# Kernel optimization log

Measured on AMD Instinct MI355X. Metric: run time of the kernel, lower is better.

## Reference

```python
import jax, jax.numpy as jnp
import numpy as np

N_NODES = 50000


def _sage_conv(x, src, dst, Wl, bl, Wr):
    # mean aggregation of source-node features into target nodes
    agg = jax.ops.segment_sum(x[src], dst, num_segments=N_NODES)      # [N, C]
    deg = jax.ops.segment_sum(jnp.ones_like(src, dtype=x.dtype), dst,
                              num_segments=N_NODES)                   # [N]
    mean = agg / jnp.maximum(deg, 1.0)[:, None]
    # PyG SAGEConv: lin_l(aggr) (with bias) + lin_r(x) (no bias)
    return mean @ Wl.T + bl + x @ Wr.T


def setup_inputs() -> dict:
    key = jax.random.key(0)
    ks = jax.random.split(key, 8)
    C = 128
    E = 600000
    scale = 1.0 / np.sqrt(C)
    x = jax.random.normal(ks[0], (N_NODES, C), dtype=jnp.float32)
    edge_index = jax.random.randint(ks[1], (2, E), 0, N_NODES, dtype=jnp.int64)
    Wl1 = jax.random.normal(ks[2], (C, C), dtype=jnp.float32) * scale
    bl1 = jnp.zeros((C,), dtype=jnp.float32)
    Wr1 = jax.random.normal(ks[3], (C, C), dtype=jnp.float32) * scale
    Wl2 = jax.random.normal(ks[4], (C, C), dtype=jnp.float32) * scale
    bl2 = jnp.zeros((C,), dtype=jnp.float32)
    Wr2 = jax.random.normal(ks[5], (C, C), dtype=jnp.float32) * scale
    return {"x": x, "edge_index": edge_index, "Wl1": Wl1, "bl1": bl1,
            "Wr1": Wr1, "Wl2": Wl2, "bl2": bl2, "Wr2": Wr2}


def reference(x, edge_index, Wl1, bl1, Wr1, Wl2, bl2, Wr2):
    src, dst = edge_index[0], edge_index[1]
    h = _sage_conv(x, src, dst, Wl1, bl1, Wr1)
    h = jax.nn.relu(h)
    out = _sage_conv(h, src, dst, Wl2, bl2, Wr2)
    return out
```

## Files before the change

### kernel.cpp

```cpp
#include <hip/hip_runtime.h>
#include <hip/hip_bf16.h>

#define N_NODES 50000
#define C 128
#define NPAD 50176
#define NTILES (NPAD / 16)
#define GEMM_BLOCKS (NTILES / 8)
#define XPREP_BLOCKS 3125
#define WPREP_BLOCKS 256
#define CAP 48

typedef short bf16x8 __attribute__((ext_vector_type(8)));
typedef float f32x4 __attribute__((ext_vector_type(4)));

__device__ __forceinline__ unsigned short f2bf(float f) {
    unsigned int u = __float_as_uint(f);
    unsigned int r = u + 0x7fffu + ((u >> 16) & 1u);
    return (unsigned short)(r >> 16);
}

__device__ __forceinline__ float bf2f(unsigned short b) {
    return __uint_as_float(((unsigned int)b) << 16);
}

__global__ __launch_bounds__(256) void buildfill_kernel(
    const int* __restrict__ src, const int* __restrict__ dst, int E, int edgeBlocks,
    int* __restrict__ cursor, int* __restrict__ csr,
    const float* __restrict__ x, unsigned short* __restrict__ Xb,
    const float* __restrict__ Wl1, const float* __restrict__ Wr1,
    const float* __restrict__ Wl2, const float* __restrict__ Wr2,
    unsigned short* __restrict__ Wc1, unsigned short* __restrict__ Wc2) {
    int b = blockIdx.x;
    if (b < edgeBlocks) {
        int e = b * 256 + threadIdx.x;
        if (e < E) {
            int d = dst[e];
            int s = src[e];
            if ((unsigned)d < (unsigned)N_NODES && (unsigned)s < (unsigned)N_NODES) {
                int slot = atomicAdd(cursor + d, 1);
                if (slot < CAP) csr[d * CAP + slot] = s;
            }
        }
    } else if (b < edgeBlocks + XPREP_BLOCKS) {
        int t = (b - edgeBlocks) * 256 + threadIdx.x;
        if (t >= N_NODES * C / 8) return;
        const float4 a = *(const float4*)(x + (size_t)t * 8);
        const float4 c = *(const float4*)(x + (size_t)t * 8 + 4);
        unsigned short o[8] = {f2bf(a.x), f2bf(a.y), f2bf(a.z), f2bf(a.w),
                               f2bf(c.x), f2bf(c.y), f2bf(c.z), f2bf(c.w)};
        *(uint4*)(Xb + (size_t)t * 8) = *(const uint4*)o;
    } else {
        int idx = (b - edgeBlocks - XPREP_BLOCKS) * 256 + threadIdx.x;
        int layer = idx >> 15;
        int r = idx & 32767;
        int j = r >> 8, k = r & 255;
        const float* Wl = layer ? Wl2 : Wl1;
        const float* Wr = layer ? Wr2 : Wr1;
        unsigned short* Wc = layer ? Wc2 : Wc1;
        float f = (k < 128) ? Wl[j * 128 + k] : Wr[j * 128 + (k - 128)];
        Wc[r] = f2bf(f);
    }
}

__global__ __launch_bounds__(256) void gather_kernel(
    const unsigned short* __restrict__ feat,
    const int* __restrict__ cursor, const int* __restrict__ csr,
    unsigned short* __restrict__ Fm) {
    int w = (blockIdx.x * 256 + threadIdx.x) >> 6;
    int lane = threadIdx.x & 63;
    if (w >= N_NODES) return;
    const int deg = min(cursor[w], CAP);
    float ax = 0.f, ay = 0.f;
    const unsigned short* fp = feat + lane * 2;
    int myidx = (lane < deg) ? csr[w * CAP + lane] : 0;
    int j = 0;
    for (; j + 7 < deg; j += 8) {
        unsigned int u[8];
#pragma unroll
        for (int l = 0; l < 8; ++l) {
            int s = __shfl(myidx, j + l);
            u[l] = *(const unsigned int*)(fp + (size_t)s * C);
        }
#pragma unroll
        for (int l = 0; l < 8; ++l) {
            ax += bf2f((unsigned short)u[l]);
            ay += bf2f((unsigned short)(u[l] >> 16));
        }
    }
    for (; j < deg; ++j) {
        int s = __shfl(myidx, j);
        unsigned int uu = *(const unsigned int*)(fp + (size_t)s * C);
        ax += bf2f((unsigned short)uu);
        ay += bf2f((unsigned short)(uu >> 16));
    }
    const float inv = 1.0f / fmaxf((float)deg, 1.0f);
    unsigned int mpack = (unsigned)f2bf(ax * inv) | ((unsigned)f2bf(ay * inv) << 16);
    *(unsigned int*)(Fm + (size_t)w * C + lane * 2) = mpack;
}

__global__ __launch_bounds__(256) void sage_gemm(
    const unsigned short* __restrict__ Fm,
    const unsigned short* __restrict__ Self,
    const unsigned short* __restrict__ Wc,
    const float* __restrict__ bias,
    void* __restrict__ outv, int relu, int obf16) {
    __shared__ unsigned short wl[128 * 264];
    for (int cidx = threadIdx.x; cidx < 4096; cidx += 256) {
        int row = cidx >> 5, chunk = cidx & 31;
        const uint4 v = *(const uint4*)(Wc + row * 256 + chunk * 8);
        *(uint4*)(&wl[row * 264 + chunk * 8]) = v;
    }
    __syncthreads();

    const int wave = threadIdx.x >> 6;
    const int lane = threadIdx.x & 63;
    const int m = lane & 15;
    const int q = lane >> 4;
    const int tile0 = blockIdx.x * 8 + wave * 2;

    const size_t rowoff = (size_t)(tile0 * 16 + m) * C + q * 8;
    const unsigned short* am = Fm + rowoff;
    const unsigned short* as = Self + rowoff;

    f32x4 acc[2][8];
#pragma unroll
    for (int t = 0; t < 2; ++t)
#pragma unroll
        for (int j = 0; j < 8; ++j) acc[t][j] = (f32x4){0.f, 0.f, 0.f, 0.f};

#pragma unroll
    for (int kt = 0; kt < 8; ++kt) {
        const unsigned short* A = (kt < 4) ? am : as;
        const int ko = (kt & 3) * 32;
        bf16x8 af0 = *(const bf16x8*)(A + ko);
        bf16x8 af1 = *(const bf16x8*)(A + 16 * C + ko);
#pragma unroll
        for (int jt = 0; jt < 8; ++jt) {
            bf16x8 bfrag = *(const bf16x8*)(&wl[(jt * 16 + m) * 264 + kt * 32 + q * 8]);
            acc[0][jt] = __builtin_amdgcn_mfma_f32_16x16x32_bf16(af0, bfrag, acc[0][jt], 0, 0, 0);
            acc[1][jt] = __builtin_amdgcn_mfma_f32_16x16x32_bf16(af1, bfrag, acc[1][jt], 0, 0, 0);
        }
    }

#pragma unroll
    for (int t = 0; t < 2; ++t) {
        int rbase = (tile0 + t) * 16 + q * 4;
#pragma unroll
        for (int r = 0; r < 4; ++r) {
            int row = rbase + r;
            if (row < N_NODES) {
#pragma unroll
                for (int jt = 0; jt < 8; ++jt) {
                    int col = jt * 16 + m;
                    float v = acc[t][jt][r] + bias[col];
                    if (relu) v = fmaxf(v, 0.0f);
                    if (obf16)
                        ((unsigned short*)outv)[(size_t)row * C + col] = f2bf(v);
                    else
                        ((float*)outv)[(size_t)row * C + col] = v;
                }
            }
        }
    }
}

extern "C" void kernel_launch(void* const* d_in, const int* in_sizes, int n_in,
                              void* d_out, int out_size, void* d_ws, size_t ws_size,
                              hipStream_t stream) {
    const float* x = (const float*)d_in[0];
    const int* edge = (const int*)d_in[1];
    const float* Wl1 = (const float*)d_in[2];
    const float* bl1 = (const float*)d_in[3];
    const float* Wr1 = (const float*)d_in[4];
    const float* Wl2 = (const float*)d_in[5];
    const float* bl2 = (const float*)d_in[6];
    const float* Wr2 = (const float*)d_in[7];
    float* out = (float*)d_out;

    const int E = in_sizes[1] / 2;
    const int* src = edge;
    const int* dst = edge + E;

    char* ws = (char*)d_ws;
    size_t off = 0;
    int* cursor = (int*)(ws + off);           off += (size_t)N_NODES * 4;
    off = (off + 511) & ~511ull;
    int* csr = (int*)(ws + off);              off += (size_t)N_NODES * CAP * 4;
    off = (off + 511) & ~511ull;
    unsigned short* Xb = (unsigned short*)(ws + off); off += (size_t)NPAD * C * 2;
    unsigned short* Fm = (unsigned short*)(ws + off); off += (size_t)NPAD * C * 2;
    unsigned short* h  = (unsigned short*)(ws + off); off += (size_t)NPAD * C * 2;
    unsigned short* Wc1 = (unsigned short*)(ws + off); off += 128 * 256 * 2;
    unsigned short* Wc2 = (unsigned short*)(ws + off); off += 128 * 256 * 2;
    (void)ws_size;

    const int edgeBlocks = (E + 255) / 256;
    const int gatherBlocks = (NPAD * 64) / 256;

    hipMemsetAsync(cursor, 0, (size_t)N_NODES * 4, stream);
    buildfill_kernel<<<edgeBlocks + XPREP_BLOCKS + WPREP_BLOCKS, 256, 0, stream>>>(
        src, dst, E, edgeBlocks, cursor, csr, x, Xb, Wl1, Wr1, Wl2, Wr2, Wc1, Wc2);

    gather_kernel<<<gatherBlocks, 256, 0, stream>>>(Xb, cursor, csr, Fm);
    sage_gemm<<<GEMM_BLOCKS, 256, 0, stream>>>(Fm, Xb, Wc1, bl1, h, 1, 1);

    gather_kernel<<<gatherBlocks, 256, 0, stream>>>(h, cursor, csr, Fm);
    sage_gemm<<<GEMM_BLOCKS, 256, 0, stream>>>(Fm, h, Wc2, bl2, out, 0, 0);
}
```

Before: 220.2 us.

## Widen gather loads to 16 bytes per lane and batch edge atomics per thread

The gather kernel now splits each wave into four groups of 16 lanes. Each group reads a full 256-byte neighbour row with uint4 loads, so four neighbours are processed in parallel, and the partial sums are combined with xor shuffles before one group writes the result. The edge-fill kernel processes four edges per thread, issuing the loads, then the atomics, then the stores in batches to expose more memory-level parallelism. The cost is more registers and shuffle reductions, and the tail handling for degrees that are not multiples of four is more complex.

```diff
diff --git a/kernel.cpp b/kernel.cpp
--- a/kernel.cpp
+++ b/kernel.cpp
@@ -9,6 +9,7 @@
 #define XPREP_BLOCKS 3125
 #define WPREP_BLOCKS 256
 #define CAP 48
+#define EPT 4
 
 typedef short bf16x8 __attribute__((ext_vector_type(8)));
 typedef float f32x4 __attribute__((ext_vector_type(4)));
@@ -21,6 +22,15 @@
 
 __device__ __forceinline__ float bf2f(unsigned short b) {
     return __uint_as_float(((unsigned int)b) << 16);
+}
+
+__device__ __forceinline__ void acc8(float* a, uint4 u) {
+    const unsigned int uu[4] = {u.x, u.y, u.z, u.w};
+#pragma unroll
+    for (int i = 0; i < 4; ++i) {
+        a[2 * i] += bf2f((unsigned short)uu[i]);
+        a[2 * i + 1] += bf2f((unsigned short)(uu[i] >> 16));
+    }
 }
 
 __global__ __launch_bounds__(256) void buildfill_kernel(
@@ -32,15 +42,26 @@
     unsigned short* __restrict__ Wc1, unsigned short* __restrict__ Wc2) {
     int b = blockIdx.x;
     if (b < edgeBlocks) {
-        int e = b * 256 + threadIdx.x;
-        if (e < E) {
-            int d = dst[e];
-            int s = src[e];
-            if ((unsigned)d < (unsigned)N_NODES && (unsigned)s < (unsigned)N_NODES) {
-                int slot = atomicAdd(cursor + d, 1);
-                if (slot < CAP) csr[d * CAP + slot] = s;
+        int e0 = b * (256 * EPT) + threadIdx.x;
+        int dd[EPT], ss[EPT], slot[EPT];
+        bool val[EPT];
+#pragma unroll
+        for (int k = 0; k < EPT; ++k) {
+            int e = e0 + k * 256;
+            val[k] = e < E;
+            if (val[k]) {
+                dd[k] = dst[e];
+                ss[k] = src[e];
+                val[k] = ((unsigned)dd[k] < (unsigned)N_NODES) &&
+                         ((unsigned)ss[k] < (unsigned)N_NODES);
             }
         }
+#pragma unroll
+        for (int k = 0; k < EPT; ++k)
+            if (val[k]) slot[k] = atomicAdd(cursor + dd[k], 1);
+#pragma unroll
+        for (int k = 0; k < EPT; ++k)
+            if (val[k] && slot[k] < CAP) csr[dd[k] * CAP + slot[k]] = ss[k];
     } else if (b < edgeBlocks + XPREP_BLOCKS) {
         int t = (b - edgeBlocks) * 256 + threadIdx.x;
         if (t >= N_NODES * C / 8) return;
@@ -70,32 +91,50 @@
     int lane = threadIdx.x & 63;
     if (w >= N_NODES) return;
     const int deg = min(cursor[w], CAP);
-    float ax = 0.f, ay = 0.f;
-    const unsigned short* fp = feat + lane * 2;
+    const int g = lane >> 4;
+    const int c = lane & 15;
+    float a[8];
+#pragma unroll
+    for (int i = 0; i < 8; ++i) a[i] = 0.f;
     int myidx = (lane < deg) ? csr[w * CAP + lane] : 0;
+    const unsigned short* fp = feat + c * 8;
     int j = 0;
-    for (; j + 7 < deg; j += 8) {
-        unsigned int u[8];
-#pragma unroll
-        for (int l = 0; l < 8; ++l) {
-            int s = __shfl(myidx, j + l);
-            u[l] = *(const unsigned int*)(fp + (size_t)s * C);
-        }
-#pragma unroll
-        for (int l = 0; l < 8; ++l) {
-            ax += bf2f((unsigned short)u[l]);
-            ay += bf2f((unsigned short)(u[l] >> 16));
-        }
-    }
-    for (; j < deg; ++j) {
-        int s = __shfl(myidx, j);
-        unsigned int uu = *(const unsigned int*)(fp + (size_t)s * C);
-        ax += bf2f((unsigned short)uu);
-        ay += bf2f((unsigned short)(uu >> 16));
+    for (; j + 8 <= deg; j += 8) {
+        int s0 = __shfl(myidx, j + g);
+        int s1 = __shfl(myidx, j + 4 + g);
+        const uint4 u0 = *(const uint4*)(fp + (size_t)s0 * C);
+        const uint4 u1 = *(const uint4*)(fp + (size_t)s1 * C);
+        acc8(a, u0);
+        acc8(a, u1);
+    }
+    if (j + 4 <= deg) {
+        int s0 = __shfl(myidx, j + g);
+        const uint4 u0 = *(const uint4*)(fp + (size_t)s0 * C);
+        acc8(a, u0);
+        j += 4;
+    }
+    int rem = deg - j;
+    if (rem) {
+        int s0 = __shfl(myidx, j + ((g < rem) ? g : 0));
+        if (g < rem) {
+            const uint4 u0 = *(const uint4*)(fp + (size_t)s0 * C);
+            acc8(a, u0);
+        }
+    }
+#pragma unroll
+    for (int i = 0; i < 8; ++i) {
+        a[i] += __shfl_xor(a[i], 16);
+        a[i] += __shfl_xor(a[i], 32);
     }
     const float inv = 1.0f / fmaxf((float)deg, 1.0f);
-    unsigned int mpack = (unsigned)f2bf(ax * inv) | ((unsigned)f2bf(ay * inv) << 16);
-    *(unsigned int*)(Fm + (size_t)w * C + lane * 2) = mpack;
+    if (g == 0) {
+        unsigned int o[4];
+#pragma unroll
+        for (int i = 0; i < 4; ++i)
+            o[i] = (unsigned)f2bf(a[2 * i] * inv) |
+                   ((unsigned)f2bf(a[2 * i + 1] * inv) << 16);
+        *(uint4*)(Fm + (size_t)w * C + c * 8) = *(const uint4*)o;
+    }
 }
 
 __global__ __launch_bounds__(256) void sage_gemm(
@@ -194,7 +233,7 @@
     unsigned short* Wc2 = (unsigned short*)(ws + off); off += 128 * 256 * 2;
     (void)ws_size;
 
-    const int edgeBlocks = (E + 255) / 256;
+    const int edgeBlocks = (E + 256 * EPT - 1) / (256 * EPT);
     const int gatherBlocks = (NPAD * 64) / 256;
 
     hipMemsetAsync(cursor, 0, (size_t)N_NODES * 4, stream);
```

Result: no change. 223.2 us (+1.4%).
